# Performance work log

Hardware: AMD Instinct MI355X
Metric: run time of the kernel (lower is better)

The kernel has to match this reference:

```python
import jax, jax.numpy as jnp
import numpy as np

NUM_CLASSES = 10
MARGIN = 1.0


def setup_inputs() -> dict:
    key = jax.random.key(0)
    k1, k2 = jax.random.split(key)
    N, D = 8192, 128
    embeddings = jax.random.normal(k1, (N, D), dtype=jnp.float32)
    labels = jax.random.randint(k2, (N,), 0, NUM_CLASSES)
    return {"embeddings": embeddings, "labels": labels}


def _batch_hard_loss(embeddings, labels):
    # embeddings: [N, D] float, labels: [N] int in [0, NUM_CLASSES)
    N = embeddings.shape[0]
    x2 = jnp.sum(embeddings * embeddings, axis=1)  # [N]
    # squared euclidean pairwise distances via gram trick, clamped at 0
    d = jnp.maximum(x2[:, None] + x2[None, :] - 2.0 * (embeddings @ embeddings.T), 0.0)  # [N, N]
    same = labels[:, None] == labels[None, :]  # [N, N]

    # hardest positive: max squared distance over same-class (includes self, as in source)
    d_pos = jnp.max(jnp.where(same, d, -jnp.inf), axis=1)  # [N]

    # FAITHFUL TO SOURCE BUG: negative_distances[k] = sum_{j: label_j != k} d(i, j)
    # = T_i - S_i(k), where S_i(k) = sum over class-k members of d(i, j)
    onehot = jax.nn.one_hot(labels, NUM_CLASSES, dtype=d.dtype)  # [N, 10]
    S = d @ onehot  # [N, 10]
    T = jnp.sum(d, axis=1)  # [N]
    neg_dist = T[:, None] - S  # [N, 10]
    k_star = jnp.argmin(neg_dist, axis=1)  # [N], values in [0, 10)

    # negatives list for class c is ordered by (class, then index); take the k_star-th element
    order = jnp.argsort(labels * N + jnp.arange(N))  # global (class, index) order
    mask_sorted = (~same)[:, order]  # [N, N] negatives of anchor i, in list order
    cs = jnp.cumsum(mask_sorted.astype(jnp.int32), axis=1)
    cond = mask_sorted & (cs == (k_star[:, None] + 1))
    pos_in_sorted = jnp.argmax(cond, axis=1)  # first position with rank k_star
    j_star = order[pos_in_sorted]  # [N] index of the "worst negative"
    d_neg = d[jnp.arange(N), j_star]  # [N]

    # base TripletLoss: relu(d_pos - d_neg + margin); mean over batch (use_gt_than_zero_mean=False)
    loss = jax.nn.relu(d_pos - d_neg + MARGIN)
    return jnp.mean(loss)


def reference(embeddings, labels):
    return _batch_hard_loss(embeddings, labels)
```

## Files before the change

kernel.cpp:

```cpp
#include <hip/hip_runtime.h>
#include <hip/hip_bf16.h>

#define BH_N 8192
#define BH_D 128
#define BH_NC 10
#define BH_MARGIN 1.0f
#define NSEG 4
#define MAXTILES (BH_N / 32 + BH_NC)
#define NCHUNK 8
#define CHROWS (BH_N / NCHUNK)

typedef __attribute__((ext_vector_type(8)))  short bf16x8;
typedef __attribute__((ext_vector_type(16))) float f32x16;

#define OFF_R(r) (((r) & 3) + 8 * ((r) >> 2))

__device__ __forceinline__ unsigned short f2bf(float f) {
    unsigned u = __float_as_uint(f);
    u += 0x7fffu + ((u >> 16) & 1u);
    return (unsigned short)(u >> 16);
}
__device__ __forceinline__ float bf2f(short h) {
    return __uint_as_float(((unsigned)(unsigned short)h) << 16);
}

__global__ __launch_bounds__(1024) void bh_prep(const float* __restrict__ E,
                                                const int* __restrict__ labels,
                                                unsigned short* __restrict__ Es,
                                                float* __restrict__ x2s,
                                                float* __restrict__ Mpart,
                                                float* __restrict__ sxpart,
                                                int* __restrict__ dposU) {
    const int t = threadIdx.x;
    const int b = blockIdx.x;
    if (b < 32) {
        const int lr = t >> 2, sub = t & 3;
        const int row = b * 256 + lr;
        const float4* ep = (const float4*)(E + (size_t)row * BH_D + sub * 32);
        float4 v[8];
#pragma unroll
        for (int k = 0; k < 8; k++) v[k] = ep[k];
        float s = 0.0f;
#pragma unroll
        for (int k = 0; k < 8; k++)
            s += v[k].x * v[k].x + v[k].y * v[k].y + v[k].z * v[k].z + v[k].w * v[k].w;
        s += __shfl_xor(s, 1); s += __shfl_xor(s, 2);
        if (sub == 0) x2s[row] = s;
        ushort4* op = (ushort4*)(Es + (size_t)row * BH_D + sub * 32);
#pragma unroll
        for (int k = 0; k < 8; k++) {
            ushort4 h;
            h.x = f2bf(v[k].x); h.y = f2bf(v[k].y); h.z = f2bf(v[k].z); h.w = f2bf(v[k].w);
            op[k] = h;
        }
        if (t < 256) dposU[b * 256 + t] = 0;
    } else {
        const int idx = b - 32;
        const int c = idx >> 3, chunk = idx & 7;
        const int lr = t >> 2, sub = t & 3;
        const int lane = t & 63;
        float acc[32];
#pragma unroll
        for (int d = 0; d < 32; d++) acc[d] = 0.0f;
        float sx = 0.0f;
#pragma unroll
        for (int rr = 0; rr < 4; rr++) {
            const int row = chunk * CHROWS + rr * 256 + lr;
            if (labels[row] == c) {
                const float4* ep = (const float4*)(E + (size_t)row * BH_D + sub * 32);
#pragma unroll
                for (int k = 0; k < 8; k++) {
                    const float4 v = ep[k];
                    acc[k * 4 + 0] += v.x; acc[k * 4 + 1] += v.y;
                    acc[k * 4 + 2] += v.z; acc[k * 4 + 3] += v.w;
                    sx += v.x * v.x + v.y * v.y + v.z * v.z + v.w * v.w;
                }
            }
        }
        __shared__ float Msh[BH_D];
        __shared__ float sxsh;
        if (t < BH_D) Msh[t] = 0.0f;
        if (t == 0) sxsh = 0.0f;
        __syncthreads();
#pragma unroll
        for (int d = 0; d < 32; d++) {
            float a = acc[d];
            a += __shfl_xor(a, 4); a += __shfl_xor(a, 8);
            a += __shfl_xor(a, 16); a += __shfl_xor(a, 32);
            if ((lane & 60) == 0) atomicAdd(&Msh[sub * 32 + d], a);
        }
        sx += __shfl_xor(sx, 1); sx += __shfl_xor(sx, 2);
        sx += __shfl_xor(sx, 4); sx += __shfl_xor(sx, 8);
        sx += __shfl_xor(sx, 16); sx += __shfl_xor(sx, 32);
        if (lane == 0) atomicAdd(&sxsh, sx);
        __syncthreads();
        if (t < BH_D) Mpart[((size_t)chunk * BH_NC + c) * BH_D + t] = Msh[t];
        if (t == 0) sxpart[chunk * BH_NC + c] = sxsh;
    }
}

__global__ __launch_bounds__(1024) void bh_sortk(const int* __restrict__ labels,
                                                 int* __restrict__ sidx,
                                                 int* __restrict__ cstart,
                                                 const float* __restrict__ Mpart,
                                                 const float* __restrict__ sxpart,
                                                 float* __restrict__ M,
                                                 float* __restrict__ sumx2,
                                                 float* __restrict__ out) {
    const int t = threadIdx.x;
    for (int i = t; i < BH_NC * BH_D; i += 1024) {
        float s = 0.0f;
#pragma unroll
        for (int ch = 0; ch < NCHUNK; ch++) s += Mpart[(size_t)ch * BH_NC * BH_D + i];
        M[i] = s;
    }
    if (t < BH_NC) {
        float s = 0.0f;
#pragma unroll
        for (int ch = 0; ch < NCHUNK; ch++) s += sxpart[ch * BH_NC + t];
        sumx2[t] = s;
    }
    if (t == 0) out[0] = 0.0f;

    const int lane = t & 63, w = t >> 6;
    const int4* lp = (const int4*)labels;
    const int4 a = lp[t * 2], b = lp[t * 2 + 1];
    int L[8] = {a.x, a.y, a.z, a.w, b.x, b.y, b.z, b.w};

    int lh[BH_NC];
#pragma unroll
    for (int c = 0; c < BH_NC; c++) lh[c] = 0;
#pragma unroll
    for (int k = 0; k < 8; k++) {
#pragma unroll
        for (int c = 0; c < BH_NC; c++) lh[c] += (L[k] == c);
    }
    int inc[BH_NC];
#pragma unroll
    for (int c = 0; c < BH_NC; c++) inc[c] = lh[c];
#pragma unroll
    for (int m = 1; m < 64; m <<= 1) {
#pragma unroll
        for (int c = 0; c < BH_NC; c++) {
            const int o = __shfl_up(inc[c], m);
            if (lane >= m) inc[c] += o;
        }
    }
    __shared__ int wtot[16][BH_NC];
    __shared__ int wpref[16][BH_NC];
    __shared__ int ctot[BH_NC];
    __shared__ int cst[BH_NC + 1];
    __shared__ int sid[BH_N];
    if (lane == 63) {
#pragma unroll
        for (int c = 0; c < BH_NC; c++) wtot[w][c] = inc[c];
    }
    __syncthreads();
    if (t < BH_NC) {
        int run = 0;
#pragma unroll
        for (int w2 = 0; w2 < 16; w2++) { wpref[w2][t] = run; run += wtot[w2][t]; }
        ctot[t] = run;
    }
    __syncthreads();
    if (t == 0) {
        int run = 0;
#pragma unroll
        for (int c = 0; c < BH_NC; c++) { cst[c] = run; run += ctot[c]; }
        cst[BH_NC] = run;
#pragma unroll
        for (int c = 0; c <= BH_NC; c++) cstart[c] = cst[c];
    }
    __syncthreads();
    int wpre[BH_NC];
#pragma unroll
    for (int c = 0; c < BH_NC; c++) wpre[c] = cst[c] + wpref[w][c] + inc[c] - lh[c];
#pragma unroll
    for (int k = 0; k < 8; k++) {
        const int j = t * 8 + k;
        const int Lk = L[k];
        int pos = 0;
#pragma unroll
        for (int c = 0; c < BH_NC; c++) pos += (Lk == c) ? wpre[c] : 0;
        sid[pos] = j;
#pragma unroll
        for (int c = 0; c < BH_NC; c++) wpre[c] += (Lk == c);
    }
    __syncthreads();
    for (int i = t; i < BH_N; i += 1024) sidx[i] = sid[i];
}

__global__ __launch_bounds__(64) void bh_dpos(const unsigned short* __restrict__ Es,
                                              const float* __restrict__ x2s,
                                              const int* __restrict__ sidx,
                                              const int* __restrict__ cstart,
                                              int* __restrict__ dposU) {
    const int tile = blockIdx.x / NSEG;
    const int seg  = blockIdx.x % NSEG;
    int cs[BH_NC + 1];
#pragma unroll
    for (int c = 0; c <= BH_NC; c++) cs[c] = cstart[c];
    int c = -1, t0 = 0, base = 0;
#pragma unroll
    for (int cc = 0; cc < BH_NC; cc++) {
        const int len = cs[cc + 1] - cs[cc];
        const int nt = (len + 31) >> 5;
        if (c < 0 && tile < base + nt) { c = cc; t0 = tile - base; }
        base += nt;
    }
    if (c < 0) return;
    const int c0 = cs[c], c1 = cs[c + 1], len = c1 - c0;
    const int rb = c0 + t0 * 32;
    const int nch = (len + 31) >> 5;
    const int per = (nch + NSEG - 1) / NSEG;
    const int jb0 = c0 + seg * per * 32;
    if (jb0 >= c1) return;
    const int jb1 = min(jb0 + per * 32, c1);

    const int lane = threadIdx.x;
    const int cid = lane & 31, half = lane >> 5;
    const int rowbase = rb + 4 * half;

    bf16x8 afrag[8];
    {
        const int ar = sidx[min(rb + cid, BH_N - 1)];
        const unsigned short* arow = Es + (size_t)ar * BH_D + half * 8;
#pragma unroll
        for (int ks = 0; ks < 8; ks++) afrag[ks] = *(const bf16x8*)(arow + ks * 16);
    }
    float xr[16];
#pragma unroll
    for (int r = 0; r < 16; r++) xr[r] = x2s[sidx[min(rowbase + OFF_R(r), BH_N - 1)]];

    float dpos[16];
#pragma unroll
    for (int r = 0; r < 16; r++) dpos[r] = 0.0f;

    int jor = sidx[min(jb0 + cid, c1 - 1)];
    bf16x8 bcur[8];
    {
        const unsigned short* brow = Es + (size_t)jor * BH_D + half * 8;
#pragma unroll
        for (int ks = 0; ks < 8; ks++) bcur[ks] = *(const bf16x8*)(brow + ks * 16);
    }
    float xc = x2s[jor];

    for (int jb = jb0; jb < jb1; jb += 32) {
        const int jorn = sidx[min(jb + 32 + cid, c1 - 1)];
        bf16x8 bnxt[8];
        {
            const unsigned short* brow = Es + (size_t)jorn * BH_D + half * 8;
#pragma unroll
            for (int ks = 0; ks < 8; ks++) bnxt[ks] = *(const bf16x8*)(brow + ks * 16);
        }
        const float xcn = x2s[jorn];

        f32x16 acc = {0.0f, 0.0f, 0.0f, 0.0f, 0.0f, 0.0f, 0.0f, 0.0f,
                      0.0f, 0.0f, 0.0f, 0.0f, 0.0f, 0.0f, 0.0f, 0.0f};
#pragma unroll
        for (int ks = 0; ks < 8; ks++)
            acc = __builtin_amdgcn_mfma_f32_32x32x16_bf16(afrag[ks], bcur[ks], acc, 0, 0, 0);

        const bool vm = (jb + cid) < jb1;
#pragma unroll
        for (int r = 0; r < 16; r++) {
            const float dd = fmaxf(fmaf(-2.0f, acc[r], xr[r] + xc), 0.0f);
            const bool rowin = (rowbase + OFF_R(r)) < c1;
            dpos[r] = fmaxf(dpos[r], (vm && rowin) ? dd : 0.0f);
        }
#pragma unroll
        for (int ks = 0; ks < 8; ks++) bcur[ks] = bnxt[ks];
        xc = xcn;
    }
#pragma unroll
    for (int r = 0; r < 16; r++) {
#pragma unroll
        for (int m = 1; m < 32; m <<= 1) dpos[r] = fmaxf(dpos[r], __shfl_xor(dpos[r], m));
    }
    if (cid == 0) {
#pragma unroll
        for (int r = 0; r < 16; r++) {
            const int row = rowbase + OFF_R(r);
            if (row < c1) atomicMax(&dposU[row], __float_as_int(dpos[r]));
        }
    }
}

__global__ __launch_bounds__(256) void bh_select(const unsigned short* __restrict__ Es,
                                                 const float* __restrict__ x2s,
                                                 const int* __restrict__ sidx,
                                                 const int* __restrict__ cstart,
                                                 const float* __restrict__ M,
                                                 const float* __restrict__ sumx2,
                                                 const int* __restrict__ dposU,
                                                 float* __restrict__ out) {
    const int w = threadIdx.x >> 6, lane = threadIdx.x & 63;
    const int spos = blockIdx.x * 4 + w;

    int cs[BH_NC + 1];
#pragma unroll
    for (int c = 0; c <= BH_NC; c++) cs[c] = cstart[c];

    const int oi = sidx[spos];
    const unsigned us0 = *(const unsigned*)(Es + (size_t)oi * BH_D + lane * 2);
    const float e0 = __uint_as_float(us0 << 16);
    const float e1 = __uint_as_float(us0 & 0xFFFF0000u);

    float dc[BH_NC];
#pragma unroll
    for (int c = 0; c < BH_NC; c++) {
        const float2 mv = *(const float2*)(M + (size_t)c * BH_D + lane * 2);
        dc[c] = e0 * mv.x + e1 * mv.y;
    }
#pragma unroll
    for (int m = 1; m < 64; m <<= 1) {
#pragma unroll
        for (int c = 0; c < BH_NC; c++) dc[c] += __shfl_xor(dc[c], m);
    }

    const float x2i = x2s[oi];
    float T = 0.0f, Sk[BH_NC];
#pragma unroll
    for (int c = 0; c < BH_NC; c++) {
        Sk[c] = (float)(cs[c + 1] - cs[c]) * x2i + sumx2[c] - 2.0f * dc[c];
        T += Sk[c];
    }
    int kstar = 0; float best = T - Sk[0];
#pragma unroll
    for (int c = 1; c < BH_NC; c++) {
        const float nd = T - Sk[c];
        if (nd < best) { best = nd; kstar = c; }
    }

    int a = 0;
#pragma unroll
    for (int c = 1; c < BH_NC; c++) a += (spos >= cs[c]);
    const int p = (kstar < cs[a]) ? kstar : (cs[a + 1] + (kstar - cs[a]));
    const int oj = sidx[p];

    const unsigned us1 = *(const unsigned*)(Es + (size_t)oj * BH_D + lane * 2);
    float dp = e0 * __uint_as_float(us1 << 16) + e1 * __uint_as_float(us1 & 0xFFFF0000u);
#pragma unroll
    for (int m = 1; m < 64; m <<= 1) dp += __shfl_xor(dp, m);
    const float dneg = fmaxf(x2i + x2s[oj] - 2.0f * dp, 0.0f);

    const float dposv = __int_as_float(dposU[spos]);
    const float loss = fmaxf(dposv - dneg + BH_MARGIN, 0.0f);

    __shared__ float ls[4];
    if (lane == 0) ls[w] = loss;
    __syncthreads();
    if (threadIdx.x == 0)
        atomicAdd(out, (ls[0] + ls[1] + ls[2] + ls[3]) * (1.0f / (float)BH_N));
}

extern "C" void kernel_launch(void* const* d_in, const int* in_sizes, int n_in,
                              void* d_out, int out_size, void* d_ws, size_t ws_size,
                              hipStream_t stream) {
    const float* E = (const float*)d_in[0];
    const int* labels = (const int*)d_in[1];
    float* out = (float*)d_out;

    unsigned short* Es = (unsigned short*)d_ws;
    float* x2s   = (float*)(Es + (size_t)BH_N * BH_D);
    float* M     = x2s + BH_N;
    float* sumx2 = M + BH_NC * BH_D;
    float* Mpart = sumx2 + 16;
    float* sxpart= Mpart + (size_t)NCHUNK * BH_NC * BH_D;
    int*   dposU = (int*)(sxpart + 128);
    int*   sidx  = dposU + BH_N;
    int*   cstart= sidx + BH_N;

    bh_prep<<<112, 1024, 0, stream>>>(E, labels, Es, x2s, Mpart, sxpart, dposU);
    bh_sortk<<<1, 1024, 0, stream>>>(labels, sidx, cstart, Mpart, sxpart, M, sumx2, out);
    bh_dpos<<<MAXTILES * NSEG, 64, 0, stream>>>(Es, x2s, sidx, cstart, dposU);
    bh_select<<<BH_N / 4, 256, 0, stream>>>(Es, x2s, sidx, cstart, M, sumx2, dposU, out);
}
```

Measured before the change: 127.2 us.

## Fold label sort into prep kernel and reduce class-mean partials in select

Removes the single-block sort kernel launch by running the counting sort as an extra block of the prep kernel. The final reduction of per-chunk class sums and squared norms moves into the select kernel, which now reads the four chunk partials directly. The chunk count is halved to keep that extra read cheap. This saves one launch and one serial single-block stage, at the cost of more redundant partial reads per warp in select and a larger shared footprint in every prep block.

```diff
diff --git a/kernel.cpp b/kernel.cpp
--- a/kernel.cpp
+++ b/kernel.cpp
@@ -7,7 +7,7 @@
 #define BH_MARGIN 1.0f
 #define NSEG 4
 #define MAXTILES (BH_N / 32 + BH_NC)
-#define NCHUNK 8
+#define NCHUNK 4
 #define CHROWS (BH_N / NCHUNK)
 
 typedef __attribute__((ext_vector_type(8)))  short bf16x8;
@@ -19,9 +19,6 @@
     unsigned u = __float_as_uint(f);
     u += 0x7fffu + ((u >> 16) & 1u);
     return (unsigned short)(u >> 16);
-}
-__device__ __forceinline__ float bf2f(short h) {
-    return __uint_as_float(((unsigned)(unsigned short)h) << 16);
 }
 
 __global__ __launch_bounds__(1024) void bh_prep(const float* __restrict__ E,
@@ -30,9 +27,13 @@
                                                 float* __restrict__ x2s,
                                                 float* __restrict__ Mpart,
                                                 float* __restrict__ sxpart,
-                                                int* __restrict__ dposU) {
+                                                int* __restrict__ dposU,
+                                                int* __restrict__ sidx,
+                                                int* __restrict__ cstart,
+                                                float* __restrict__ out) {
     const int t = threadIdx.x;
     const int b = blockIdx.x;
+    __shared__ int sid[BH_N];
     if (b < 32) {
         const int lr = t >> 2, sub = t & 3;
         const int row = b * 256 + lr;
@@ -54,9 +55,9 @@
             op[k] = h;
         }
         if (t < 256) dposU[b * 256 + t] = 0;
-    } else {
+    } else if (b < 72) {
         const int idx = b - 32;
-        const int c = idx >> 3, chunk = idx & 7;
+        const int c = idx >> 2, chunk = idx & 3;
         const int lr = t >> 2, sub = t & 3;
         const int lane = t & 63;
         float acc[32];
@@ -64,7 +65,7 @@
         for (int d = 0; d < 32; d++) acc[d] = 0.0f;
         float sx = 0.0f;
 #pragma unroll
-        for (int rr = 0; rr < 4; rr++) {
+        for (int rr = 0; rr < 8; rr++) {
             const int row = chunk * CHROWS + rr * 256 + lr;
             if (labels[row] == c) {
                 const float4* ep = (const float4*)(E + (size_t)row * BH_D + sub * 32);
@@ -77,10 +78,10 @@
                 }
             }
         }
-        __shared__ float Msh[BH_D];
-        __shared__ float sxsh;
+        float* Msh = (float*)sid;
+        float* sxsh = Msh + BH_D;
         if (t < BH_D) Msh[t] = 0.0f;
-        if (t == 0) sxsh = 0.0f;
+        if (t == 0) sxsh[0] = 0.0f;
         __syncthreads();
 #pragma unroll
         for (int d = 0; d < 32; d++) {
@@ -92,102 +93,78 @@
         sx += __shfl_xor(sx, 1); sx += __shfl_xor(sx, 2);
         sx += __shfl_xor(sx, 4); sx += __shfl_xor(sx, 8);
         sx += __shfl_xor(sx, 16); sx += __shfl_xor(sx, 32);
-        if (lane == 0) atomicAdd(&sxsh, sx);
+        if (lane == 0) atomicAdd(&sxsh[0], sx);
         __syncthreads();
         if (t < BH_D) Mpart[((size_t)chunk * BH_NC + c) * BH_D + t] = Msh[t];
-        if (t == 0) sxpart[chunk * BH_NC + c] = sxsh;
-    }
-}
-
-__global__ __launch_bounds__(1024) void bh_sortk(const int* __restrict__ labels,
-                                                 int* __restrict__ sidx,
-                                                 int* __restrict__ cstart,
-                                                 const float* __restrict__ Mpart,
-                                                 const float* __restrict__ sxpart,
-                                                 float* __restrict__ M,
-                                                 float* __restrict__ sumx2,
-                                                 float* __restrict__ out) {
-    const int t = threadIdx.x;
-    for (int i = t; i < BH_NC * BH_D; i += 1024) {
-        float s = 0.0f;
-#pragma unroll
-        for (int ch = 0; ch < NCHUNK; ch++) s += Mpart[(size_t)ch * BH_NC * BH_D + i];
-        M[i] = s;
-    }
-    if (t < BH_NC) {
-        float s = 0.0f;
-#pragma unroll
-        for (int ch = 0; ch < NCHUNK; ch++) s += sxpart[ch * BH_NC + t];
-        sumx2[t] = s;
-    }
-    if (t == 0) out[0] = 0.0f;
-
-    const int lane = t & 63, w = t >> 6;
-    const int4* lp = (const int4*)labels;
-    const int4 a = lp[t * 2], b = lp[t * 2 + 1];
-    int L[8] = {a.x, a.y, a.z, a.w, b.x, b.y, b.z, b.w};
-
-    int lh[BH_NC];
-#pragma unroll
-    for (int c = 0; c < BH_NC; c++) lh[c] = 0;
-#pragma unroll
-    for (int k = 0; k < 8; k++) {
-#pragma unroll
-        for (int c = 0; c < BH_NC; c++) lh[c] += (L[k] == c);
-    }
-    int inc[BH_NC];
-#pragma unroll
-    for (int c = 0; c < BH_NC; c++) inc[c] = lh[c];
-#pragma unroll
-    for (int m = 1; m < 64; m <<= 1) {
-#pragma unroll
-        for (int c = 0; c < BH_NC; c++) {
-            const int o = __shfl_up(inc[c], m);
-            if (lane >= m) inc[c] += o;
-        }
-    }
-    __shared__ int wtot[16][BH_NC];
-    __shared__ int wpref[16][BH_NC];
-    __shared__ int ctot[BH_NC];
-    __shared__ int cst[BH_NC + 1];
-    __shared__ int sid[BH_N];
-    if (lane == 63) {
-#pragma unroll
-        for (int c = 0; c < BH_NC; c++) wtot[w][c] = inc[c];
-    }
-    __syncthreads();
-    if (t < BH_NC) {
-        int run = 0;
-#pragma unroll
-        for (int w2 = 0; w2 < 16; w2++) { wpref[w2][t] = run; run += wtot[w2][t]; }
-        ctot[t] = run;
-    }
-    __syncthreads();
-    if (t == 0) {
-        int run = 0;
-#pragma unroll
-        for (int c = 0; c < BH_NC; c++) { cst[c] = run; run += ctot[c]; }
-        cst[BH_NC] = run;
-#pragma unroll
-        for (int c = 0; c <= BH_NC; c++) cstart[c] = cst[c];
-    }
-    __syncthreads();
-    int wpre[BH_NC];
-#pragma unroll
-    for (int c = 0; c < BH_NC; c++) wpre[c] = cst[c] + wpref[w][c] + inc[c] - lh[c];
-#pragma unroll
-    for (int k = 0; k < 8; k++) {
-        const int j = t * 8 + k;
-        const int Lk = L[k];
-        int pos = 0;
-#pragma unroll
-        for (int c = 0; c < BH_NC; c++) pos += (Lk == c) ? wpre[c] : 0;
-        sid[pos] = j;
-#pragma unroll
-        for (int c = 0; c < BH_NC; c++) wpre[c] += (Lk == c);
-    }
-    __syncthreads();
-    for (int i = t; i < BH_N; i += 1024) sidx[i] = sid[i];
+        if (t == 0) sxpart[chunk * BH_NC + c] = sxsh[0];
+    } else {
+        if (t == 0) out[0] = 0.0f;
+        const int lane = t & 63, w = t >> 6;
+        const int4* lp = (const int4*)labels;
+        const int4 a = lp[t * 2], bb = lp[t * 2 + 1];
+        int L[8] = {a.x, a.y, a.z, a.w, bb.x, bb.y, bb.z, bb.w};
+
+        int lh[BH_NC];
+#pragma unroll
+        for (int c = 0; c < BH_NC; c++) lh[c] = 0;
+#pragma unroll
+        for (int k = 0; k < 8; k++) {
+#pragma unroll
+            for (int c = 0; c < BH_NC; c++) lh[c] += (L[k] == c);
+        }
+        int inc[BH_NC];
+#pragma unroll
+        for (int c = 0; c < BH_NC; c++) inc[c] = lh[c];
+#pragma unroll
+        for (int m = 1; m < 64; m <<= 1) {
+#pragma unroll
+            for (int c = 0; c < BH_NC; c++) {
+                const int o = __shfl_up(inc[c], m);
+                if (lane >= m) inc[c] += o;
+            }
+        }
+        __shared__ int wtot[16][BH_NC];
+        __shared__ int wpref[16][BH_NC];
+        __shared__ int ctot[BH_NC];
+        __shared__ int cst[BH_NC + 1];
+        if (lane == 63) {
+#pragma unroll
+            for (int c = 0; c < BH_NC; c++) wtot[w][c] = inc[c];
+        }
+        __syncthreads();
+        if (t < BH_NC) {
+            int run = 0;
+#pragma unroll
+            for (int w2 = 0; w2 < 16; w2++) { wpref[w2][t] = run; run += wtot[w2][t]; }
+            ctot[t] = run;
+        }
+        __syncthreads();
+        if (t == 0) {
+            int run = 0;
+#pragma unroll
+            for (int c = 0; c < BH_NC; c++) { cst[c] = run; run += ctot[c]; }
+            cst[BH_NC] = run;
+#pragma unroll
+            for (int c = 0; c <= BH_NC; c++) cstart[c] = cst[c];
+        }
+        __syncthreads();
+        int wpre[BH_NC];
+#pragma unroll
+        for (int c = 0; c < BH_NC; c++) wpre[c] = cst[c] + wpref[w][c] + inc[c] - lh[c];
+#pragma unroll
+        for (int k = 0; k < 8; k++) {
+            const int j = t * 8 + k;
+            const int Lk = L[k];
+            int pos = 0;
+#pragma unroll
+            for (int c = 0; c < BH_NC; c++) pos += (Lk == c) ? wpre[c] : 0;
+            sid[pos] = j;
+#pragma unroll
+            for (int c = 0; c < BH_NC; c++) wpre[c] += (Lk == c);
+        }
+        __syncthreads();
+        for (int i = t; i < BH_N; i += 1024) sidx[i] = sid[i];
+    }
 }
 
 __global__ __launch_bounds__(64) void bh_dpos(const unsigned short* __restrict__ Es,
@@ -290,8 +267,8 @@
                                                  const float* __restrict__ x2s,
                                                  const int* __restrict__ sidx,
                                                  const int* __restrict__ cstart,
-                                                 const float* __restrict__ M,
-                                                 const float* __restrict__ sumx2,
+                                                 const float* __restrict__ Mpart,
+                                                 const float* __restrict__ sxpart,
                                                  const int* __restrict__ dposU,
                                                  float* __restrict__ out) {
     const int w = threadIdx.x >> 6, lane = threadIdx.x & 63;
@@ -309,8 +286,13 @@
     float dc[BH_NC];
 #pragma unroll
     for (int c = 0; c < BH_NC; c++) {
-        const float2 mv = *(const float2*)(M + (size_t)c * BH_D + lane * 2);
-        dc[c] = e0 * mv.x + e1 * mv.y;
+        float d = 0.0f;
+#pragma unroll
+        for (int ch = 0; ch < NCHUNK; ch++) {
+            const float2 mv = *(const float2*)(Mpart + ((size_t)ch * BH_NC + c) * BH_D + lane * 2);
+            d += e0 * mv.x + e1 * mv.y;
+        }
+        dc[c] = d;
     }
 #pragma unroll
     for (int m = 1; m < 64; m <<= 1) {
@@ -322,7 +304,10 @@
     float T = 0.0f, Sk[BH_NC];
 #pragma unroll
     for (int c = 0; c < BH_NC; c++) {
-        Sk[c] = (float)(cs[c + 1] - cs[c]) * x2i + sumx2[c] - 2.0f * dc[c];
+        float sx2 = 0.0f;
+#pragma unroll
+        for (int ch = 0; ch < NCHUNK; ch++) sx2 += sxpart[ch * BH_NC + c];
+        Sk[c] = (float)(cs[c + 1] - cs[c]) * x2i + sx2 - 2.0f * dc[c];
         T += Sk[c];
     }
     int kstar = 0; float best = T - Sk[0];
@@ -363,16 +348,13 @@
 
     unsigned short* Es = (unsigned short*)d_ws;
     float* x2s   = (float*)(Es + (size_t)BH_N * BH_D);
-    float* M     = x2s + BH_N;
-    float* sumx2 = M + BH_NC * BH_D;
-    float* Mpart = sumx2 + 16;
+    float* Mpart = x2s + BH_N;
     float* sxpart= Mpart + (size_t)NCHUNK * BH_NC * BH_D;
     int*   dposU = (int*)(sxpart + 128);
     int*   sidx  = dposU + BH_N;
     int*   cstart= sidx + BH_N;
 
-    bh_prep<<<112, 1024, 0, stream>>>(E, labels, Es, x2s, Mpart, sxpart, dposU);
-    bh_sortk<<<1, 1024, 0, stream>>>(labels, sidx, cstart, Mpart, sxpart, M, sumx2, out);
+    bh_prep<<<73, 1024, 0, stream>>>(E, labels, Es, x2s, Mpart, sxpart, dposU, sidx, cstart, out);
     bh_dpos<<<MAXTILES * NSEG, 64, 0, stream>>>(Es, x2s, sidx, cstart, dposU);
-    bh_select<<<BH_N / 4, 256, 0, stream>>>(Es, x2s, sidx, cstart, M, sumx2, dposU, out);
-}
+    bh_select<<<BH_N / 4, 256, 0, stream>>>(Es, x2s, sidx, cstart, Mpart, sxpart, dposU, out);
+}
```

After: 124.0 us. 2.5% less time.
